# Performance work log

Hardware: AMD Instinct MI355X
Metric: run time of the kernel (lower is better)

The kernel has to match this reference:

```python
import jax, jax.numpy as jnp
import numpy as np

N_NODES = 50000
N_EDGES = 800000
IN_F, HID_F, OUT_F = 256, 128, 64
NEG_SLOPE = 0.2
EPS = 1e-16


def _aggregate_with_attention(x, src, tgt, a_w, a_b, num_nodes):
    # x: [N, d]; src/tgt: [E]; a_w: [2d]; a_b: [1]
    d = x.shape[-1]
    x_src = x[src]                                   # [E, d] gather
    # att(cat([x_src, x_tgt])) == x_src @ a_w[:d] + x_tgt @ a_w[d:] + b
    alpha = x_src @ a_w[:d] + x[tgt] @ a_w[d:] + a_b[0]   # [E]
    alpha = jnp.where(alpha >= 0, alpha, NEG_SLOPE * alpha)  # leaky_relu(0.2)
    # segment softmax over edges grouped by target node
    m = jax.ops.segment_max(alpha, tgt, num_segments=num_nodes)   # [N]
    e = jnp.exp(alpha - m[tgt])                                    # [E]
    s = jax.ops.segment_sum(e, tgt, num_segments=num_nodes)       # [N]
    alpha = e / (s[tgt] + EPS)                                     # [E]
    msgs = x_src * alpha[:, None]                                  # [E, d]
    return jax.ops.segment_sum(msgs, tgt, num_segments=num_nodes)  # [N, d]


def setup_inputs() -> dict:
    key = jax.random.key(0)
    ks = jax.random.split(key, 10)
    x = jax.random.normal(ks[0], (N_NODES, IN_F), dtype=jnp.float32)
    edge_index = jax.random.randint(ks[1], (2, N_EDGES), 0, N_NODES, dtype=jnp.int32)
    sc1 = 1.0 / np.sqrt(IN_F)
    sc2 = 1.0 / np.sqrt(HID_F)
    return {
        "x": x,
        "edge_index": edge_index,
        "W1": jax.random.normal(ks[2], (IN_F, HID_F), dtype=jnp.float32) * sc1,
        "b1": jax.random.normal(ks[3], (HID_F,), dtype=jnp.float32) * sc1,
        "a1_w": jax.random.normal(ks[4], (2 * HID_F,), dtype=jnp.float32) * sc2,
        "a1_b": jax.random.normal(ks[5], (1,), dtype=jnp.float32) * sc2,
        "W2": jax.random.normal(ks[6], (HID_F, OUT_F), dtype=jnp.float32) * sc2,
        "b2": jax.random.normal(ks[7], (OUT_F,), dtype=jnp.float32) * sc2,
        "a2_w": jax.random.normal(ks[8], (2 * OUT_F,), dtype=jnp.float32) * (1.0 / np.sqrt(OUT_F)),
        "a2_b": jax.random.normal(ks[9], (1,), dtype=jnp.float32) * (1.0 / np.sqrt(OUT_F)),
    }


def reference(x, edge_index, W1, b1, a1_w, a1_b, W2, b2, a2_w, a2_b):
    src, tgt = edge_index[0], edge_index[1]
    n = x.shape[0]
    # eval mode: dropout is identity
    h = jax.nn.elu(x @ W1 + b1)                           # [N, HID]
    h = _aggregate_with_attention(h, src, tgt, a1_w, a1_b, n)
    o = h @ W2 + b2                                        # [N, OUT]
    o = _aggregate_with_attention(o, src, tgt, a2_w, a2_b, n)
    return jax.nn.log_softmax(o, axis=-1)
```

## Files before the change

kernel.cpp:

```cpp
#include <hip/hip_runtime.h>

#define NN    50000
#define NE    800000
#define INF_  256
#define HIDF  128
#define OUTF  64
#define NBUCK 196
#define CAP   5120
#define CHUNK 2048

typedef unsigned int uint;
typedef unsigned short ushort;
typedef __attribute__((ext_vector_type(8))) short short8;
typedef __attribute__((ext_vector_type(4))) float float4v;

__device__ __forceinline__ short f2bf(float f) {
    union { float f; unsigned u; } v; v.f = f;
    unsigned r = v.u + 0x7fffu + ((v.u >> 16) & 1u);
    return (short)(r >> 16);
}
__device__ __forceinline__ float bflo(uint u) {
    union { uint u; float f; } v; v.u = u << 16; return v.f;
}
__device__ __forceinline__ float bfhi(uint u) {
    union { uint u; float f; } v; v.u = u & 0xffff0000u; return v.f;
}

__device__ __forceinline__ int excl_scan256(int v, int* ws) {
    int lane = threadIdx.x & 63, wv = threadIdx.x >> 6;
    int x = v;
    #pragma unroll
    for (int o = 1; o < 64; o <<= 1) {
        int y = __shfl_up(x, o);
        if (lane >= o) x += y;
    }
    if (lane == 63) ws[wv] = x;
    __syncthreads();
    int add = 0;
    #pragma unroll
    for (int w = 0; w < 4; w++) add += (w < wv) ? ws[w] : 0;
    return x + add - v;
}

__global__ __launch_bounds__(256) void k_prep(const float* __restrict__ W1, const float* __restrict__ W2,
                                              short* __restrict__ W1f, short* __restrict__ W2f) {
    int i = blockIdx.x * 256 + threadIdx.x;
    if (i < INF_ * HIDF) {
        int kk = i & 7, t = i >> 3;
        int m_l = t & 15, q = (t >> 4) & 3, s = t >> 6;
        int nb = s & 7, kc = s >> 3;
        int k = kc * 32 + q * 8 + kk, n = nb * 16 + m_l;
        W1f[i] = f2bf(W1[k * HIDF + n]);
    } else if (i < INF_ * HIDF + HIDF * OUTF) {
        int i2 = i - INF_ * HIDF;
        int kk = i2 & 7, t = i2 >> 3;
        int m_l = t & 15, q = (t >> 4) & 3, s = t >> 6;
        int nb = s & 3, kc = s >> 2;
        int k = kc * 32 + q * 8 + kk, n = nb * 16 + m_l;
        W2f[i2] = f2bf(W2[k * OUTF + n]);
    }
}


__global__ __launch_bounds__(256) void k_part1(const int* __restrict__ src, const int* __restrict__ tgt,
                                               int* __restrict__ bcur, uint2* __restrict__ pairs) {
    __shared__ int hist[NBUCK], lofs[NBUCK], cur[NBUCK], gstart[NBUCK];
    __shared__ int ws[4];
    __shared__ int ltgt[CHUNK], lsrc[CHUNK];
    int tid = threadIdx.x;
    for (int i = tid; i < NBUCK; i += 256) hist[i] = 0;
    __syncthreads();

    int base = blockIdx.x * CHUNK;
    int cnt = NE - base; if (cnt > CHUNK) cnt = CHUNK;

    int t_[8], s_[8];
    #pragma unroll
    for (int k = 0; k < 8; k++) {
        int idx = k * 256 + tid;
        if (idx < cnt) {
            int j = base + idx;
            t_[k] = tgt[j]; s_[k] = src[j];
            atomicAdd(&hist[t_[k] >> 8], 1);
        } else t_[k] = -1;
    }
    __syncthreads();

    int v = (tid < NBUCK) ? hist[tid] : 0;
    int excl = excl_scan256(v, ws);
    if (tid < NBUCK) {
        lofs[tid] = excl;
        cur[tid] = excl;
        gstart[tid] = atomicAdd(&bcur[tid], v);
    }
    __syncthreads();

    #pragma unroll
    for (int k = 0; k < 8; k++) {
        if (t_[k] >= 0) {
            int b = t_[k] >> 8;
            int pos = atomicAdd(&cur[b], 1);
            ltgt[pos] = t_[k]; lsrc[pos] = s_[k];
        }
    }
    __syncthreads();

    for (int j = tid; j < cnt; j += 256) {
        int tv = ltgt[j];
        int b = tv >> 8;
        int dst = gstart[b] + (j - lofs[b]);
        pairs[(size_t)b * CAP + dst] = make_uint2((uint)tv, (uint)lsrc[j]);
    }
}

__global__ __launch_bounds__(256) void k_part2(const int* __restrict__ bcur, const uint2* __restrict__ pairs,
                                               int* __restrict__ fsrc, int* __restrict__ nbeg,
                                               int* __restrict__ ncnt) {
    __shared__ int hist[256], cur[256];
    __shared__ int ws[4];
    __shared__ ushort lt[CAP];
    __shared__ int ls[CAP], ss_[CAP];
    int tid = threadIdx.x;
    int b = blockIdx.x;
    int cnt = __builtin_amdgcn_readfirstlane(bcur[b]);
    hist[tid] = 0;
    __syncthreads();

    const uint2* pb = pairs + (size_t)b * CAP;
    for (int j = tid; j < cnt; j += 256) {
        uint2 e = pb[j];
        int fine = e.x & 255;
        lt[j] = (ushort)fine; ls[j] = (int)e.y;
        atomicAdd(&hist[fine], 1);
    }
    __syncthreads();

    int v = hist[tid];
    int excl = excl_scan256(v, ws);
    int node = (b << 8) + tid;
    if (node < NN) { nbeg[node] = b * CAP + excl; ncnt[node] = v; }
    cur[tid] = excl;
    __syncthreads();

    for (int j = tid; j < cnt; j += 256) {
        int pos = atomicAdd(&cur[lt[j]], 1);
        ss_[pos] = ls[j];
    }
    __syncthreads();

    for (int j = tid; j < cnt; j += 256)
        fsrc[(size_t)b * CAP + j] = ss_[j];
}


__global__ __launch_bounds__(256) void k_linear1(const float* __restrict__ X, const short* __restrict__ W1f,
                                                 const float* __restrict__ b1, ushort* __restrict__ Hb) {
    int w = threadIdx.x >> 6;
    int l = threadIdx.x & 63;
    int m_l = l & 15, q = l >> 4;
    int row0 = blockIdx.x * 64 + w * 16;
    int rA0 = row0 + m_l;
    int rc0 = rA0 < NN ? rA0 : NN - 1;
    const float* pa0 = X + (size_t)rc0 * INF_ + q * 8;
    const short8* Bp = (const short8*)W1f;

    float4v acc[8] = {};
    #pragma unroll
    for (int kc = 0; kc < 8; kc++) {
        int k0 = kc * 32;
        float4 u0 = *(const float4*)(pa0 + k0);
        float4 u1 = *(const float4*)(pa0 + k0 + 4);
        short8 a0;
        a0[0] = f2bf(u0.x); a0[1] = f2bf(u0.y); a0[2] = f2bf(u0.z); a0[3] = f2bf(u0.w);
        a0[4] = f2bf(u1.x); a0[5] = f2bf(u1.y); a0[6] = f2bf(u1.z); a0[7] = f2bf(u1.w);
        #pragma unroll
        for (int n = 0; n < 8; n++) {
            short8 b = Bp[(kc * 8 + n) * 64 + l];
            acc[n] = __builtin_amdgcn_mfma_f32_16x16x32_bf16(a0, b, acc[n], 0, 0, 0);
        }
    }

    #pragma unroll
    for (int n = 0; n < 8; n++) {
        int col = n * 16 + m_l;
        float bias = b1[col];
        #pragma unroll
        for (int r = 0; r < 4; r++) {
            int row = row0 + q * 4 + r;
            if (row < NN) {
                float v = acc[n][r] + bias;
                v = v > 0.f ? v : expm1f(v);
                Hb[(size_t)row * HIDF + col] = (ushort)f2bf(v);
            }
        }
    }
}

__global__ __launch_bounds__(256) void k_linear2(const short* __restrict__ Hin, const short* __restrict__ W2f,
                                                 const float* __restrict__ b2, ushort* __restrict__ Ob) {
    int w = threadIdx.x >> 6;
    int l = threadIdx.x & 63;
    int m_l = l & 15, q = l >> 4;
    int row0 = blockIdx.x * 64 + w * 16;
    int rA0 = row0 + m_l;
    int rc0 = rA0 < NN ? rA0 : NN - 1;
    const short* pa0 = Hin + (size_t)rc0 * HIDF + q * 8;
    const short8* Bp = (const short8*)W2f;

    float4v acc[4] = {};
    #pragma unroll
    for (int kc = 0; kc < 4; kc++) {
        int k0 = kc * 32;
        short8 a0 = *(const short8*)(pa0 + k0);
        #pragma unroll
        for (int n = 0; n < 4; n++) {
            short8 b = Bp[(kc * 4 + n) * 64 + l];
            acc[n] = __builtin_amdgcn_mfma_f32_16x16x32_bf16(a0, b, acc[n], 0, 0, 0);
        }
    }

    #pragma unroll
    for (int n = 0; n < 4; n++) {
        int col = n * 16 + m_l;
        float bias = b2[col];
        #pragma unroll
        for (int r = 0; r < 4; r++) {
            int row = row0 + q * 4 + r;
            if (row < NN)
                Ob[(size_t)row * OUTF + col] = (ushort)f2bf(acc[n][r] + bias);
        }
    }
}


__global__ __launch_bounds__(256) void k_s1(const uint* __restrict__ Hb4, const float* __restrict__ a1w,
                                            float* __restrict__ s1s, float* __restrict__ s1t) {
    int wid  = (blockIdx.x * 256 + threadIdx.x) >> 6;
    int lane = threadIdx.x & 63;
    if (wid >= NN) return;
    uint h = Hb4[(size_t)wid * 64 + lane];
    float h0 = bflo(h), h1 = bfhi(h);
    float2 as = ((const float2*)a1w)[lane];
    float2 at = ((const float2*)(a1w + HIDF))[lane];
    float vs = h0 * as.x + h1 * as.y;
    float vt = h0 * at.x + h1 * at.y;
    #pragma unroll
    for (int o = 32; o > 0; o >>= 1) { vs += __shfl_xor(vs, o); vt += __shfl_xor(vt, o); }
    if (lane == 0) { s1s[wid] = vs; s1t[wid] = vt; }
}

__global__ __launch_bounds__(256) void k_s2(const uint* __restrict__ Ob4, const float* __restrict__ a2w,
                                            float* __restrict__ s2s, float* __restrict__ s2t) {
    int wid = (blockIdx.x * 256 + threadIdx.x) >> 5;
    int li  = threadIdx.x & 31;
    if (wid >= NN) return;
    uint o = Ob4[(size_t)wid * 32 + li];
    float v0 = bflo(o), v1 = bfhi(o);
    float2 as = ((const float2*)a2w)[li];
    float2 at = ((const float2*)(a2w + OUTF))[li];
    float vs = v0 * as.x + v1 * as.y;
    float vt = v0 * at.x + v1 * at.y;
    #pragma unroll
    for (int o2 = 16; o2 > 0; o2 >>= 1) { vs += __shfl_xor(vs, o2); vt += __shfl_xor(vt, o2); }
    if (li == 0) { s2s[wid] = vs; s2t[wid] = vt; }
}


__global__ __launch_bounds__(256) void k_agg1f(const uint* __restrict__ Hb4, const int* __restrict__ nbeg,
                                               const int* __restrict__ ncnt, const int* __restrict__ fsrc,
                                               const float* __restrict__ ss, const float* __restrict__ st_,
                                               const float* __restrict__ ab, uint* __restrict__ Hagg4) {
    int wid  = (blockIdx.x * 256 + threadIdx.x) >> 6;
    int lane = threadIdx.x & 63;
    if (wid >= NN) return;
    int beg = __builtin_amdgcn_readfirstlane(nbeg[wid]);
    int deg = __builtin_amdgcn_readfirstlane(ncnt[wid]);
    int end = beg + deg;
    float bias = ab[0] + st_[wid];
    float ax = 0.f, ay = 0.f, bx = 0.f, by = 0.f;

    if (deg > 0 && deg <= 64) {
        int my_s = 0; float a = -INFINITY;
        if (lane < deg) {
            my_s = fsrc[beg + lane];
            float t = ss[my_s] + bias;
            a = t >= 0.f ? t : 0.2f * t;
        }
        float m = a;
        #pragma unroll
        for (int o = 32; o > 0; o >>= 1) m = fmaxf(m, __shfl_xor(m, o));
        float e = (lane < deg) ? __expf(a - m) : 0.f;
        float sum = e;
        #pragma unroll
        for (int o = 32; o > 0; o >>= 1) sum += __shfl_xor(sum, o);
        float p = e * (1.f / (sum + 1e-16f));
        for (int j = 0; j < deg; j += 4) {
            int s0 = __shfl(my_s, j),     s1 = __shfl(my_s, j + 1);
            int s2 = __shfl(my_s, j + 2), s3 = __shfl(my_s, j + 3);
            float w0 = __shfl(p, j),     w1 = __shfl(p, j + 1);
            float w2 = __shfl(p, j + 2), w3 = __shfl(p, j + 3);
            uint x0 = Hb4[(size_t)s0 * 64 + lane];
            uint x1 = Hb4[(size_t)s1 * 64 + lane];
            uint x2 = Hb4[(size_t)s2 * 64 + lane];
            uint x3 = Hb4[(size_t)s3 * 64 + lane];
            ax += w0 * bflo(x0); ay += w0 * bfhi(x0);
            bx += w1 * bflo(x1); by += w1 * bfhi(x1);
            ax += w2 * bflo(x2); ay += w2 * bfhi(x2);
            bx += w3 * bflo(x3); by += w3 * bfhi(x3);
        }
    } else if (deg > 64) {
        float m = -INFINITY;
        for (int i = beg + lane; i < end; i += 64) {
            float t = ss[fsrc[i]] + bias;
            t = t >= 0.f ? t : 0.2f * t;
            m = fmaxf(m, t);
        }
        #pragma unroll
        for (int o = 32; o > 0; o >>= 1) m = fmaxf(m, __shfl_xor(m, o));
        float sum = 0.f;
        for (int i = beg + lane; i < end; i += 64) {
            float t = ss[fsrc[i]] + bias;
            t = t >= 0.f ? t : 0.2f * t;
            sum += __expf(t - m);
        }
        #pragma unroll
        for (int o = 32; o > 0; o >>= 1) sum += __shfl_xor(sum, o);
        float inv = 1.f / (sum + 1e-16f);
        for (int c = beg; c < end; c += 64) {
            int cnt = min(64, end - c);
            int my_s = 0; float p = 0.f;
            if (lane < cnt) {
                my_s = fsrc[c + lane];
                float t = ss[my_s] + bias;
                t = t >= 0.f ? t : 0.2f * t;
                p = __expf(t - m) * inv;
            }
            for (int j = 0; j < cnt; j += 4) {
                int s0 = __shfl(my_s, j),     s1 = __shfl(my_s, j + 1);
                int s2 = __shfl(my_s, j + 2), s3 = __shfl(my_s, j + 3);
                float w0 = __shfl(p, j),     w1 = __shfl(p, j + 1);
                float w2 = __shfl(p, j + 2), w3 = __shfl(p, j + 3);
                uint x0 = Hb4[(size_t)s0 * 64 + lane];
                uint x1 = Hb4[(size_t)s1 * 64 + lane];
                uint x2 = Hb4[(size_t)s2 * 64 + lane];
                uint x3 = Hb4[(size_t)s3 * 64 + lane];
                ax += w0 * bflo(x0); ay += w0 * bfhi(x0);
                bx += w1 * bflo(x1); by += w1 * bfhi(x1);
                ax += w2 * bflo(x2); ay += w2 * bfhi(x2);
                bx += w3 * bflo(x3); by += w3 * bfhi(x3);
            }
        }
    }
    float fx = ax + bx, fy = ay + by;
    uint outv = (uint)(ushort)f2bf(fx) | ((uint)(ushort)f2bf(fy) << 16);
    Hagg4[(size_t)wid * 64 + lane] = outv;
}

__global__ __launch_bounds__(256) void k_agg2f(const uint* __restrict__ Ob4, const int* __restrict__ nbeg,
                                               const int* __restrict__ ncnt, const int* __restrict__ fsrc,
                                               const float* __restrict__ ss, const float* __restrict__ st_,
                                               const float* __restrict__ ab, float* __restrict__ out) {
    int wid  = (blockIdx.x * 256 + threadIdx.x) >> 6;
    int lane = threadIdx.x & 63;
    if (wid >= NN) return;
    int half = lane >> 5, li = lane & 31;
    int beg = __builtin_amdgcn_readfirstlane(nbeg[wid]);
    int deg = __builtin_amdgcn_readfirstlane(ncnt[wid]);
    int end = beg + deg;
    float bias = ab[0] + st_[wid];
    float a0 = 0.f, a1 = 0.f;

    if (deg > 0 && deg <= 64) {
        int my_s = 0; float a = -INFINITY;
        if (lane < deg) {
            my_s = fsrc[beg + lane];
            float t = ss[my_s] + bias;
            a = t >= 0.f ? t : 0.2f * t;
        }
        float m = a;
        #pragma unroll
        for (int o = 32; o > 0; o >>= 1) m = fmaxf(m, __shfl_xor(m, o));
        float e = (lane < deg) ? __expf(a - m) : 0.f;
        float sum = e;
        #pragma unroll
        for (int o = 32; o > 0; o >>= 1) sum += __shfl_xor(sum, o);
        float p = e * (1.f / (sum + 1e-16f));
        for (int j = 0; j < deg; j += 4) {
            int e0 = j + half, e1 = j + 2 + half;
            int s0 = __shfl(my_s, e0), s1 = __shfl(my_s, e1);
            float w0 = __shfl(p, e0), w1 = __shfl(p, e1);
            uint x0 = Ob4[(size_t)s0 * 32 + li];
            uint x1 = Ob4[(size_t)s1 * 32 + li];
            a0 += w0 * bflo(x0); a1 += w0 * bfhi(x0);
            a0 += w1 * bflo(x1); a1 += w1 * bfhi(x1);
        }
    } else if (deg > 64) {
        float m = -INFINITY;
        for (int i = beg + lane; i < end; i += 64) {
            float t = ss[fsrc[i]] + bias;
            t = t >= 0.f ? t : 0.2f * t;
            m = fmaxf(m, t);
        }
        #pragma unroll
        for (int o = 32; o > 0; o >>= 1) m = fmaxf(m, __shfl_xor(m, o));
        float sum = 0.f;
        for (int i = beg + lane; i < end; i += 64) {
            float t = ss[fsrc[i]] + bias;
            t = t >= 0.f ? t : 0.2f * t;
            sum += __expf(t - m);
        }
        #pragma unroll
        for (int o = 32; o > 0; o >>= 1) sum += __shfl_xor(sum, o);
        float inv = 1.f / (sum + 1e-16f);
        for (int c = beg; c < end; c += 64) {
            int cnt = min(64, end - c);
            int my_s = 0; float p = 0.f;
            if (lane < cnt) {
                my_s = fsrc[c + lane];
                float t = ss[my_s] + bias;
                t = t >= 0.f ? t : 0.2f * t;
                p = __expf(t - m) * inv;
            }
            for (int j = 0; j < cnt; j += 4) {
                int e0 = j + half, e1 = j + 2 + half;
                int s0 = __shfl(my_s, e0), s1 = __shfl(my_s, e1);
                float w0 = __shfl(p, e0), w1 = __shfl(p, e1);
                uint x0 = Ob4[(size_t)s0 * 32 + li];
                uint x1 = Ob4[(size_t)s1 * 32 + li];
                a0 += w0 * bflo(x0); a1 += w0 * bfhi(x0);
                a0 += w1 * bflo(x1); a1 += w1 * bfhi(x1);
            }
        }
    }
    a0 += __shfl_xor(a0, 32);
    a1 += __shfl_xor(a1, 32);
    float mx = fmaxf(a0, a1);
    #pragma unroll
    for (int o = 16; o > 0; o >>= 1) mx = fmaxf(mx, __shfl_xor(mx, o));
    float es = __expf(a0 - mx) + __expf(a1 - mx);
    #pragma unroll
    for (int o = 16; o > 0; o >>= 1) es += __shfl_xor(es, o);
    float lg = __logf(es);
    if (half == 0) {
        float2 r; r.x = a0 - mx - lg; r.y = a1 - mx - lg;
        ((float2*)out)[(size_t)wid * 32 + li] = r;
    }
}


extern "C" void kernel_launch(void* const* d_in, const int* in_sizes, int n_in,
                              void* d_out, int out_size, void* d_ws, size_t ws_size,
                              hipStream_t stream) {
    const float* X   = (const float*)d_in[0];
    const int*   ei  = (const int*)d_in[1];
    const float* W1  = (const float*)d_in[2];
    const float* b1  = (const float*)d_in[3];
    const float* a1w = (const float*)d_in[4];
    const float* a1b = (const float*)d_in[5];
    const float* W2  = (const float*)d_in[6];
    const float* b2  = (const float*)d_in[7];
    const float* a2w = (const float*)d_in[8];
    const float* a2b = (const float*)d_in[9];
    const int* src = ei;
    const int* tgt = ei + NE;

    char* p = (char*)d_ws;
    size_t off = 0;
    auto alloc = [&](size_t bytes) -> char* {
        char* r = p + off;
        off = (off + bytes + 255) & ~(size_t)255;
        return r;
    };
    ushort* Hb    = (ushort*)alloc((size_t)NN * HIDF * 2);
    ushort* Hagg  = (ushort*)alloc((size_t)NN * HIDF * 2);
    ushort* Ob    = (ushort*)alloc((size_t)NN * OUTF * 2);
    short* W1f    = (short*)alloc((size_t)INF_ * HIDF * 2);
    short* W2f    = (short*)alloc((size_t)HIDF * OUTF * 2);
    float* s1s    = (float*)alloc((size_t)NN * 4);
    float* s1t    = (float*)alloc((size_t)NN * 4);
    float* s2s    = (float*)alloc((size_t)NN * 4);
    float* s2t    = (float*)alloc((size_t)NN * 4);
    int*   bcur   = (int*)alloc((size_t)NBUCK * 4);
    uint2* pairs  = (uint2*)alloc((size_t)NBUCK * CAP * 8);
    int*   fsrc   = (int*)alloc((size_t)NBUCK * CAP * 4);
    int*   nbeg   = (int*)alloc((size_t)NN * 4);
    int*   ncnt   = (int*)alloc((size_t)NN * 4);

    hipMemsetAsync(bcur, 0, (size_t)NBUCK * 4, stream);
    k_prep   <<<(INF_ * HIDF + HIDF * OUTF + 255) / 256, 256, 0, stream>>>(W1, W2, W1f, W2f);
    k_part1  <<<(NE + CHUNK - 1) / CHUNK, 256, 0, stream>>>(src, tgt, bcur, pairs);
    k_part2  <<<NBUCK, 256, 0, stream>>>(bcur, pairs, fsrc, nbeg, ncnt);

    k_linear1<<<(NN + 63) / 64, 256, 0, stream>>>(X, W1f, b1, Hb);
    k_s1     <<<NN / 4, 256, 0, stream>>>((const uint*)Hb, a1w, s1s, s1t);
    k_agg1f  <<<NN / 4, 256, 0, stream>>>((const uint*)Hb, nbeg, ncnt, fsrc, s1s, s1t, a1b, (uint*)Hagg);

    k_linear2<<<(NN + 63) / 64, 256, 0, stream>>>((const short*)Hagg, W2f, b2, Ob);
    k_s2     <<<NN / 8, 256, 0, stream>>>((const uint*)Ob, a2w, s2s, s2t);
    k_agg2f  <<<NN / 4, 256, 0, stream>>>((const uint*)Ob, nbeg, ncnt, fsrc, s2s, s2t, a2b, (float*)d_out);
}
```

Baseline: 237.4 us.

## Fuse partitioning with linear1, fold attention scores into GEMMs, unroll gathers

Runs the edge bucketing and the first linear layer as independent block ranges of one kernel, and folds the bucket-counter reset into k_prep instead of a memset. Computes the per-node source and target attention scores in the GEMM epilogues with a shuffle reduction, which removes the separate k_s1 and k_s2 kernels and their re-reads of H and O. It also simplifies k_part2 to scatter straight to global memory without LDS staging, and unrolls the neighbor gathers in both aggregation kernels to 8 edges per iteration for more loads in flight. The cost is fewer launches and less memory traffic, in exchange for higher register pressure, scores computed from fp32 values rather than bf16-rounded ones, and non-coalesced fsrc writes in part2.

```diff
diff --git a/kernel.cpp b/kernel.cpp
--- a/kernel.cpp
+++ b/kernel.cpp
@@ -8,6 +8,9 @@
 #define NBUCK 196
 #define CAP   5120
 #define CHUNK 2048
+#define NPART1 ((NE + CHUNK - 1) / CHUNK)
+#define NLIN1  ((NN + 63) / 64)
+#define NPREP  160
 
 typedef unsigned int uint;
 typedef unsigned short ushort;
@@ -43,7 +46,12 @@
 }
 
 __global__ __launch_bounds__(256) void k_prep(const float* __restrict__ W1, const float* __restrict__ W2,
-                                              short* __restrict__ W1f, short* __restrict__ W2f) {
+                                              short* __restrict__ W1f, short* __restrict__ W2f,
+                                              int* __restrict__ bcur) {
+    if (blockIdx.x == NPREP) {
+        if (threadIdx.x < NBUCK) bcur[threadIdx.x] = 0;
+        return;
+    }
     int i = blockIdx.x * 256 + threadIdx.x;
     if (i < INF_ * HIDF) {
         int kk = i & 7, t = i >> 3;
@@ -62,103 +70,67 @@
 }
 
 
-__global__ __launch_bounds__(256) void k_part1(const int* __restrict__ src, const int* __restrict__ tgt,
-                                               int* __restrict__ bcur, uint2* __restrict__ pairs) {
-    __shared__ int hist[NBUCK], lofs[NBUCK], cur[NBUCK], gstart[NBUCK];
-    __shared__ int ws[4];
-    __shared__ int ltgt[CHUNK], lsrc[CHUNK];
-    int tid = threadIdx.x;
-    for (int i = tid; i < NBUCK; i += 256) hist[i] = 0;
-    __syncthreads();
-
-    int base = blockIdx.x * CHUNK;
-    int cnt = NE - base; if (cnt > CHUNK) cnt = CHUNK;
-
-    int t_[8], s_[8];
-    #pragma unroll
-    for (int k = 0; k < 8; k++) {
-        int idx = k * 256 + tid;
-        if (idx < cnt) {
-            int j = base + idx;
-            t_[k] = tgt[j]; s_[k] = src[j];
-            atomicAdd(&hist[t_[k] >> 8], 1);
-        } else t_[k] = -1;
-    }
-    __syncthreads();
-
-    int v = (tid < NBUCK) ? hist[tid] : 0;
-    int excl = excl_scan256(v, ws);
-    if (tid < NBUCK) {
-        lofs[tid] = excl;
-        cur[tid] = excl;
-        gstart[tid] = atomicAdd(&bcur[tid], v);
-    }
-    __syncthreads();
-
-    #pragma unroll
-    for (int k = 0; k < 8; k++) {
-        if (t_[k] >= 0) {
-            int b = t_[k] >> 8;
-            int pos = atomicAdd(&cur[b], 1);
-            ltgt[pos] = t_[k]; lsrc[pos] = s_[k];
-        }
-    }
-    __syncthreads();
-
-    for (int j = tid; j < cnt; j += 256) {
-        int tv = ltgt[j];
-        int b = tv >> 8;
-        int dst = gstart[b] + (j - lofs[b]);
-        pairs[(size_t)b * CAP + dst] = make_uint2((uint)tv, (uint)lsrc[j]);
-    }
-}
-
-__global__ __launch_bounds__(256) void k_part2(const int* __restrict__ bcur, const uint2* __restrict__ pairs,
-                                               int* __restrict__ fsrc, int* __restrict__ nbeg,
-                                               int* __restrict__ ncnt) {
-    __shared__ int hist[256], cur[256];
-    __shared__ int ws[4];
-    __shared__ ushort lt[CAP];
-    __shared__ int ls[CAP], ss_[CAP];
-    int tid = threadIdx.x;
-    int b = blockIdx.x;
-    int cnt = __builtin_amdgcn_readfirstlane(bcur[b]);
-    hist[tid] = 0;
-    __syncthreads();
-
-    const uint2* pb = pairs + (size_t)b * CAP;
-    for (int j = tid; j < cnt; j += 256) {
-        uint2 e = pb[j];
-        int fine = e.x & 255;
-        lt[j] = (ushort)fine; ls[j] = (int)e.y;
-        atomicAdd(&hist[fine], 1);
-    }
-    __syncthreads();
-
-    int v = hist[tid];
-    int excl = excl_scan256(v, ws);
-    int node = (b << 8) + tid;
-    if (node < NN) { nbeg[node] = b * CAP + excl; ncnt[node] = v; }
-    cur[tid] = excl;
-    __syncthreads();
-
-    for (int j = tid; j < cnt; j += 256) {
-        int pos = atomicAdd(&cur[lt[j]], 1);
-        ss_[pos] = ls[j];
-    }
-    __syncthreads();
-
-    for (int j = tid; j < cnt; j += 256)
-        fsrc[(size_t)b * CAP + j] = ss_[j];
-}
-
-
-__global__ __launch_bounds__(256) void k_linear1(const float* __restrict__ X, const short* __restrict__ W1f,
-                                                 const float* __restrict__ b1, ushort* __restrict__ Hb) {
+__global__ __launch_bounds__(256, 3) void k_f1(const int* __restrict__ src, const int* __restrict__ tgt,
+                                               int* __restrict__ bcur, uint2* __restrict__ pairs,
+                                               const float* __restrict__ X, const short* __restrict__ W1f,
+                                               const float* __restrict__ b1, ushort* __restrict__ Hb,
+                                               const float* __restrict__ a1w, float* __restrict__ s1s,
+                                               float* __restrict__ s1t) {
+    if (blockIdx.x < NPART1) {
+        __shared__ int hist[NBUCK], lofs[NBUCK], cur[NBUCK], gstart[NBUCK];
+        __shared__ int ws[4];
+        __shared__ int ltgt[CHUNK], lsrc[CHUNK];
+        int tid = threadIdx.x;
+        for (int i = tid; i < NBUCK; i += 256) hist[i] = 0;
+        __syncthreads();
+
+        int base = blockIdx.x * CHUNK;
+        int cnt = NE - base; if (cnt > CHUNK) cnt = CHUNK;
+
+        int t_[8], s_[8];
+        #pragma unroll
+        for (int k = 0; k < 8; k++) {
+            int idx = k * 256 + tid;
+            if (idx < cnt) {
+                int j = base + idx;
+                t_[k] = tgt[j]; s_[k] = src[j];
+                atomicAdd(&hist[t_[k] >> 8], 1);
+            } else t_[k] = -1;
+        }
+        __syncthreads();
+
+        int v = (tid < NBUCK) ? hist[tid] : 0;
+        int excl = excl_scan256(v, ws);
+        if (tid < NBUCK) {
+            lofs[tid] = excl;
+            cur[tid] = excl;
+            gstart[tid] = atomicAdd(&bcur[tid], v);
+        }
+        __syncthreads();
+
+        #pragma unroll
+        for (int k = 0; k < 8; k++) {
+            if (t_[k] >= 0) {
+                int b = t_[k] >> 8;
+                int pos = atomicAdd(&cur[b], 1);
+                ltgt[pos] = t_[k]; lsrc[pos] = s_[k];
+            }
+        }
+        __syncthreads();
+
+        for (int j = tid; j < cnt; j += 256) {
+            int tv = ltgt[j];
+            int b = tv >> 8;
+            int dst = gstart[b] + (j - lofs[b]);
+            pairs[(size_t)b * CAP + dst] = make_uint2((uint)tv, (uint)lsrc[j]);
+        }
+        return;
+    }
+    int bid = blockIdx.x - NPART1;
     int w = threadIdx.x >> 6;
     int l = threadIdx.x & 63;
     int m_l = l & 15, q = l >> 4;
-    int row0 = blockIdx.x * 64 + w * 16;
+    int row0 = bid * 64 + w * 16;
     int rA0 = row0 + m_l;
     int rc0 = rA0 < NN ? rA0 : NN - 1;
     const float* pa0 = X + (size_t)rc0 * INF_ + q * 8;
@@ -180,24 +152,74 @@
         }
     }
 
+    float vs_r[4] = {0.f, 0.f, 0.f, 0.f}, vt_r[4] = {0.f, 0.f, 0.f, 0.f};
     #pragma unroll
     for (int n = 0; n < 8; n++) {
         int col = n * 16 + m_l;
         float bias = b1[col];
+        float aw0 = a1w[col], aw1 = a1w[HIDF + col];
         #pragma unroll
         for (int r = 0; r < 4; r++) {
             int row = row0 + q * 4 + r;
-            if (row < NN) {
-                float v = acc[n][r] + bias;
-                v = v > 0.f ? v : expm1f(v);
-                Hb[(size_t)row * HIDF + col] = (ushort)f2bf(v);
-            }
-        }
-    }
-}
-
-__global__ __launch_bounds__(256) void k_linear2(const short* __restrict__ Hin, const short* __restrict__ W2f,
-                                                 const float* __restrict__ b2, ushort* __restrict__ Ob) {
+            float v = acc[n][r] + bias;
+            v = v > 0.f ? v : expm1f(v);
+            vs_r[r] += v * aw0; vt_r[r] += v * aw1;
+            if (row < NN) Hb[(size_t)row * HIDF + col] = (ushort)f2bf(v);
+        }
+    }
+    #pragma unroll
+    for (int r = 0; r < 4; r++) {
+        #pragma unroll
+        for (int o = 1; o < 16; o <<= 1) {
+            vs_r[r] += __shfl_xor(vs_r[r], o);
+            vt_r[r] += __shfl_xor(vt_r[r], o);
+        }
+    }
+    if (m_l == 0) {
+        #pragma unroll
+        for (int r = 0; r < 4; r++) {
+            int row = row0 + q * 4 + r;
+            if (row < NN) { s1s[row] = vs_r[r]; s1t[row] = vt_r[r]; }
+        }
+    }
+}
+
+__global__ __launch_bounds__(256) void k_part2(const int* __restrict__ bcur, const uint2* __restrict__ pairs,
+                                               int* __restrict__ fsrc, int* __restrict__ nbeg,
+                                               int* __restrict__ ncnt) {
+    __shared__ int hist[256], cur[256];
+    __shared__ int ws[4];
+    int tid = threadIdx.x;
+    int b = blockIdx.x;
+    int cnt = __builtin_amdgcn_readfirstlane(bcur[b]);
+    hist[tid] = 0;
+    __syncthreads();
+
+    const uint2* pb = pairs + (size_t)b * CAP;
+    for (int j = tid; j < cnt; j += 256) {
+        uint2 e = pb[j];
+        atomicAdd(&hist[e.x & 255], 1);
+    }
+    __syncthreads();
+
+    int v = hist[tid];
+    int excl = excl_scan256(v, ws);
+    int node = (b << 8) + tid;
+    if (node < NN) { nbeg[node] = b * CAP + excl; ncnt[node] = v; }
+    cur[tid] = excl;
+    __syncthreads();
+
+    for (int j = tid; j < cnt; j += 256) {
+        uint2 e = pb[j];
+        int pos = atomicAdd(&cur[e.x & 255], 1);
+        fsrc[(size_t)b * CAP + pos] = (int)e.y;
+    }
+}
+
+__global__ __launch_bounds__(256, 3) void k_linear2(const short* __restrict__ Hin, const short* __restrict__ W2f,
+                                                    const float* __restrict__ b2, ushort* __restrict__ Ob,
+                                                    const float* __restrict__ a2w, float* __restrict__ s2s,
+                                                    float* __restrict__ s2t) {
     int w = threadIdx.x >> 6;
     int l = threadIdx.x & 63;
     int m_l = l & 15, q = l >> 4;
@@ -219,50 +241,35 @@
         }
     }
 
+    float vs_r[4] = {0.f, 0.f, 0.f, 0.f}, vt_r[4] = {0.f, 0.f, 0.f, 0.f};
     #pragma unroll
     for (int n = 0; n < 4; n++) {
         int col = n * 16 + m_l;
         float bias = b2[col];
+        float aw0 = a2w[col], aw1 = a2w[OUTF + col];
         #pragma unroll
         for (int r = 0; r < 4; r++) {
             int row = row0 + q * 4 + r;
-            if (row < NN)
-                Ob[(size_t)row * OUTF + col] = (ushort)f2bf(acc[n][r] + bias);
-        }
-    }
-}
-
-
-__global__ __launch_bounds__(256) void k_s1(const uint* __restrict__ Hb4, const float* __restrict__ a1w,
-                                            float* __restrict__ s1s, float* __restrict__ s1t) {
-    int wid  = (blockIdx.x * 256 + threadIdx.x) >> 6;
-    int lane = threadIdx.x & 63;
-    if (wid >= NN) return;
-    uint h = Hb4[(size_t)wid * 64 + lane];
-    float h0 = bflo(h), h1 = bfhi(h);
-    float2 as = ((const float2*)a1w)[lane];
-    float2 at = ((const float2*)(a1w + HIDF))[lane];
-    float vs = h0 * as.x + h1 * as.y;
-    float vt = h0 * at.x + h1 * at.y;
-    #pragma unroll
-    for (int o = 32; o > 0; o >>= 1) { vs += __shfl_xor(vs, o); vt += __shfl_xor(vt, o); }
-    if (lane == 0) { s1s[wid] = vs; s1t[wid] = vt; }
-}
-
-__global__ __launch_bounds__(256) void k_s2(const uint* __restrict__ Ob4, const float* __restrict__ a2w,
-                                            float* __restrict__ s2s, float* __restrict__ s2t) {
-    int wid = (blockIdx.x * 256 + threadIdx.x) >> 5;
-    int li  = threadIdx.x & 31;
-    if (wid >= NN) return;
-    uint o = Ob4[(size_t)wid * 32 + li];
-    float v0 = bflo(o), v1 = bfhi(o);
-    float2 as = ((const float2*)a2w)[li];
-    float2 at = ((const float2*)(a2w + OUTF))[li];
-    float vs = v0 * as.x + v1 * as.y;
-    float vt = v0 * at.x + v1 * at.y;
-    #pragma unroll
-    for (int o2 = 16; o2 > 0; o2 >>= 1) { vs += __shfl_xor(vs, o2); vt += __shfl_xor(vt, o2); }
-    if (li == 0) { s2s[wid] = vs; s2t[wid] = vt; }
+            float v = acc[n][r] + bias;
+            vs_r[r] += v * aw0; vt_r[r] += v * aw1;
+            if (row < NN) Ob[(size_t)row * OUTF + col] = (ushort)f2bf(v);
+        }
+    }
+    #pragma unroll
+    for (int r = 0; r < 4; r++) {
+        #pragma unroll
+        for (int o = 1; o < 16; o <<= 1) {
+            vs_r[r] += __shfl_xor(vs_r[r], o);
+            vt_r[r] += __shfl_xor(vt_r[r], o);
+        }
+    }
+    if (m_l == 0) {
+        #pragma unroll
+        for (int r = 0; r < 4; r++) {
+            int row = row0 + q * 4 + r;
+            if (row < NN) { s2s[row] = vs_r[r]; s2t[row] = vt_r[r]; }
+        }
+    }
 }
 
 
@@ -294,19 +301,17 @@
         #pragma unroll
         for (int o = 32; o > 0; o >>= 1) sum += __shfl_xor(sum, o);
         float p = e * (1.f / (sum + 1e-16f));
-        for (int j = 0; j < deg; j += 4) {
-            int s0 = __shfl(my_s, j),     s1 = __shfl(my_s, j + 1);
-            int s2 = __shfl(my_s, j + 2), s3 = __shfl(my_s, j + 3);
-            float w0 = __shfl(p, j),     w1 = __shfl(p, j + 1);
-            float w2 = __shfl(p, j + 2), w3 = __shfl(p, j + 3);
-            uint x0 = Hb4[(size_t)s0 * 64 + lane];
-            uint x1 = Hb4[(size_t)s1 * 64 + lane];
-            uint x2 = Hb4[(size_t)s2 * 64 + lane];
-            uint x3 = Hb4[(size_t)s3 * 64 + lane];
-            ax += w0 * bflo(x0); ay += w0 * bfhi(x0);
-            bx += w1 * bflo(x1); by += w1 * bfhi(x1);
-            ax += w2 * bflo(x2); ay += w2 * bfhi(x2);
-            bx += w3 * bflo(x3); by += w3 * bfhi(x3);
+        for (int j = 0; j < deg; j += 8) {
+            int sA[8]; float wA[8]; uint xA[8];
+            #pragma unroll
+            for (int u = 0; u < 8; u++) { sA[u] = __shfl(my_s, j + u); wA[u] = __shfl(p, j + u); }
+            #pragma unroll
+            for (int u = 0; u < 8; u++) xA[u] = Hb4[(size_t)sA[u] * 64 + lane];
+            #pragma unroll
+            for (int u = 0; u < 8; u += 2) {
+                ax += wA[u] * bflo(xA[u]);     ay += wA[u] * bfhi(xA[u]);
+                bx += wA[u + 1] * bflo(xA[u + 1]); by += wA[u + 1] * bfhi(xA[u + 1]);
+            }
         }
     } else if (deg > 64) {
         float m = -INFINITY;
@@ -385,14 +390,20 @@
         #pragma unroll
         for (int o = 32; o > 0; o >>= 1) sum += __shfl_xor(sum, o);
         float p = e * (1.f / (sum + 1e-16f));
-        for (int j = 0; j < deg; j += 4) {
-            int e0 = j + half, e1 = j + 2 + half;
+        for (int j = 0; j < deg; j += 8) {
+            int e0 = j + half, e1 = j + 2 + half, e2 = j + 4 + half, e3 = j + 6 + half;
             int s0 = __shfl(my_s, e0), s1 = __shfl(my_s, e1);
+            int s2 = __shfl(my_s, e2), s3 = __shfl(my_s, e3);
             float w0 = __shfl(p, e0), w1 = __shfl(p, e1);
+            float w2 = __shfl(p, e2), w3 = __shfl(p, e3);
             uint x0 = Ob4[(size_t)s0 * 32 + li];
             uint x1 = Ob4[(size_t)s1 * 32 + li];
+            uint x2 = Ob4[(size_t)s2 * 32 + li];
+            uint x3 = Ob4[(size_t)s3 * 32 + li];
             a0 += w0 * bflo(x0); a1 += w0 * bfhi(x0);
             a0 += w1 * bflo(x1); a1 += w1 * bfhi(x1);
+            a0 += w2 * bflo(x2); a1 += w2 * bfhi(x2);
+            a0 += w3 * bflo(x3); a1 += w3 * bfhi(x3);
         }
     } else if (deg > 64) {
         float m = -INFINITY;
@@ -486,16 +497,11 @@
     int*   nbeg   = (int*)alloc((size_t)NN * 4);
     int*   ncnt   = (int*)alloc((size_t)NN * 4);
 
-    hipMemsetAsync(bcur, 0, (size_t)NBUCK * 4, stream);
-    k_prep   <<<(INF_ * HIDF + HIDF * OUTF + 255) / 256, 256, 0, stream>>>(W1, W2, W1f, W2f);
-    k_part1  <<<(NE + CHUNK - 1) / CHUNK, 256, 0, stream>>>(src, tgt, bcur, pairs);
+    k_prep   <<<NPREP + 1, 256, 0, stream>>>(W1, W2, W1f, W2f, bcur);
+    k_f1     <<<NPART1 + NLIN1, 256, 0, stream>>>(src, tgt, bcur, pairs,
+                                                  X, W1f, b1, Hb, a1w, s1s, s1t);
     k_part2  <<<NBUCK, 256, 0, stream>>>(bcur, pairs, fsrc, nbeg, ncnt);
-
-    k_linear1<<<(NN + 63) / 64, 256, 0, stream>>>(X, W1f, b1, Hb);
-    k_s1     <<<NN / 4, 256, 0, stream>>>((const uint*)Hb, a1w, s1s, s1t);
     k_agg1f  <<<NN / 4, 256, 0, stream>>>((const uint*)Hb, nbeg, ncnt, fsrc, s1s, s1t, a1b, (uint*)Hagg);
-
-    k_linear2<<<(NN + 63) / 64, 256, 0, stream>>>((const short*)Hagg, W2f, b2, Ob);
-    k_s2     <<<NN / 8, 256, 0, stream>>>((const uint*)Ob, a2w, s2s, s2t);
+    k_linear2<<<NLIN1, 256, 0, stream>>>((const short*)Hagg, W2f, b2, Ob, a2w, s2s, s2t);
     k_agg2f  <<<NN / 4, 256, 0, stream>>>((const uint*)Ob, nbeg, ncnt, fsrc, s2s, s2t, a2b, (float*)d_out);
 }
```

New measurement: 212.5 us. 10.5% less time.
